# Performance work log

Hardware: AMD Instinct MI355X
Metric: run time of the kernel (lower is better)

Reference implementation:

```python
import jax, jax.numpy as jnp
import numpy as np

N = 50000      # nodes
E = 800000     # edges (before self-loops)
IN = 128       # in_channels
HID = 64       # hidden_channels
HEADS = 4      # num_heads of gat1
ACT = 5        # num_actions
NEG_SLOPE = 0.2


def gat_conv(x, edge_index, W, a_src, a_dst, bias, heads, out_ch):
    """PyG-style GATConv (concat=True, add_self_loops=True, eval mode)."""
    n = x.shape[0]
    loops = jnp.arange(n)
    src = jnp.concatenate([edge_index[0], loops])  # messages flow src -> dst
    dst = jnp.concatenate([edge_index[1], loops])
    h = (x @ W).reshape(n, heads, out_ch)                 # [N,H,C]
    alpha_src = jnp.sum(h * a_src, axis=-1)               # [N,H]
    alpha_dst = jnp.sum(h * a_dst, axis=-1)               # [N,H]
    e = jax.nn.leaky_relu(alpha_src[src] + alpha_dst[dst], NEG_SLOPE)  # [Et,H]
    # numerically-stable segment softmax over incoming edges of each dst node
    e_max = jax.lax.stop_gradient(jax.ops.segment_max(e, dst, num_segments=n))
    e_max = jnp.where(jnp.isfinite(e_max), e_max, 0.0)
    p = jnp.exp(e - e_max[dst])                           # [Et,H]
    denom = jax.ops.segment_sum(p, dst, num_segments=n)   # [N,H]
    alpha = p / (denom[dst] + 1e-16)                      # [Et,H]
    out = jax.ops.segment_sum(h[src] * alpha[:, :, None], dst, num_segments=n)
    return out.reshape(n, heads * out_ch) + bias


def setup_inputs() -> dict:
    key = jax.random.key(0)
    ks = jax.random.split(key, 12)
    s = 0.1
    return {
        "x": jax.random.normal(ks[0], (N, IN), jnp.float32),
        "edge_index": jax.random.randint(ks[1], (2, E), 0, N, dtype=jnp.int32),
        "W1": jax.random.normal(ks[2], (IN, HEADS * HID), jnp.float32) * s,
        "a1_src": jax.random.normal(ks[3], (HEADS, HID), jnp.float32) * s,
        "a1_dst": jax.random.normal(ks[4], (HEADS, HID), jnp.float32) * s,
        "b1": jnp.zeros((HEADS * HID,), jnp.float32),
        "W2": jax.random.normal(ks[5], (HEADS * HID, HID), jnp.float32) * s,
        "a2_src": jax.random.normal(ks[6], (1, HID), jnp.float32) * s,
        "a2_dst": jax.random.normal(ks[7], (1, HID), jnp.float32) * s,
        "b2": jnp.zeros((HID,), jnp.float32),
        "Wfc": jax.random.normal(ks[8], (HID, ACT), jnp.float32) * s,
        "bfc": jnp.zeros((ACT,), jnp.float32),
    }


def reference(x, edge_index, W1, a1_src, a1_dst, b1, W2, a2_src, a2_dst, b2, Wfc, bfc):
    # x.view(-1, F) is a no-op for already-flat [N, F] input; dropout skipped (eval).
    h = jax.nn.relu(gat_conv(x, edge_index, W1, a1_src, a1_dst, b1, HEADS, HID))
    h = jax.nn.relu(gat_conv(h, edge_index, W2, a2_src, a2_dst, b2, 1, HID))
    return h @ Wfc + bfc  # [N, num_actions]
```

## Files before the change

kernel.cpp:

```cpp
#include <hip/hip_runtime.h>

#define NEG_SLOPE 0.2f
#define ELLW 32

__device__ __forceinline__ float leaky(float x) { return x > 0.f ? x : NEG_SLOPE * x; }

__device__ __forceinline__ void unpack2(unsigned u, float& lo, float& hi) {
    union { unsigned u; float f; } a, b;
    a.u = u << 16; b.u = u & 0xffff0000u;
    lo = a.f; hi = b.f;
}

__device__ __forceinline__ unsigned short f2bf(float f) {
    unsigned u = __float_as_uint(f);
    u += 0x7fffu + ((u >> 16) & 1u);
    return (unsigned short)(u >> 16);
}

__global__ void k_count(const int* __restrict__ dst, int E, int* __restrict__ cnt) {
    int i = blockIdx.x * blockDim.x + threadIdx.x;
    if (i < E) atomicAdd(&cnt[dst[i]], 1);
}

__global__ __launch_bounds__(256) void k_scanA(const int* __restrict__ cnt, int* __restrict__ rowptr,
                                               int* __restrict__ bsum, int n) {
    int b = blockIdx.x, t = threadIdx.x;
    int lane = t & 63, w = t >> 6;
    int i0 = b * 1024 + t * 4;
    int v0 = (i0 + 0 < n) ? cnt[i0 + 0] : 0;
    int v1 = (i0 + 1 < n) ? cnt[i0 + 1] : 0;
    int v2 = (i0 + 2 < n) ? cnt[i0 + 2] : 0;
    int v3 = (i0 + 3 < n) ? cnt[i0 + 3] : 0;
    int r0 = v0, r1 = r0 + v1, r2 = r1 + v2, r3 = r2 + v3;
    int s = r3;
    int q = s;
    #pragma unroll
    for (int off = 1; off < 64; off <<= 1) {
        int tval = __shfl_up(q, off);
        if (lane >= off) q += tval;
    }
    __shared__ int wsum[4];
    if (lane == 63) wsum[w] = q;
    __syncthreads();
    int woff = 0;
    #pragma unroll
    for (int k = 0; k < 4; k++) if (k < w) woff += wsum[k];
    int excl = woff + q - s;
    if (i0 + 0 < n) rowptr[1 + i0 + 0] = excl + r0;
    if (i0 + 1 < n) rowptr[1 + i0 + 1] = excl + r1;
    if (i0 + 2 < n) rowptr[1 + i0 + 2] = excl + r2;
    if (i0 + 3 < n) rowptr[1 + i0 + 3] = excl + r3;
    if (t == 255) bsum[b] = woff + q;
}

__global__ void k_scanB(const int* __restrict__ bsum, int* __restrict__ bscan, int nb) {
    int lane = threadIdx.x & 63;
    int v = (lane < nb) ? bsum[lane] : 0;
    #pragma unroll
    for (int off = 1; off < 64; off <<= 1) {
        int t = __shfl_up(v, off);
        if (lane >= off) v += t;
    }
    if (lane < nb) bscan[lane] = v;
}

__global__ __launch_bounds__(256) void k_scanC(int* __restrict__ rowptr, const int* __restrict__ bscan, int n) {
    int b = blockIdx.x, t = threadIdx.x;
    int i0 = b * 1024 + t * 4;
    if (b == 0) {
        if (t == 0) rowptr[0] = 0;
        return;
    }
    int add = bscan[b - 1];
    #pragma unroll
    for (int j = 0; j < 4; j++)
        if (i0 + j < n) rowptr[1 + i0 + j] += add;
}

__global__ void k_copy(const int* __restrict__ src, int* __restrict__ dst, int n) {
    int i = blockIdx.x * blockDim.x + threadIdx.x;
    if (i < n) dst[i] = src[i];
}

__global__ void k_scatter(const int* __restrict__ srcn, const int* __restrict__ dstn, int E,
                          const int* __restrict__ rowptr, int* __restrict__ wptr,
                          int* __restrict__ col, int* __restrict__ ell) {
    int i = blockIdx.x * blockDim.x + threadIdx.x;
    if (i < E) {
        int d = dstn[i];
        int s = srcn[i];
        int pos = atomicAdd(&wptr[d], 1);
        col[pos] = s;
        int slot = pos - rowptr[d];
        if (slot < ELLW) ell[(size_t)d * ELLW + slot] = s;
    }
}

template <int BMT, bool WF32, bool WBF16, bool FALPHA>
__global__ __launch_bounds__(256) void k_gemm(const float* __restrict__ A, const float* __restrict__ B,
                                              float* __restrict__ C, unsigned short* __restrict__ Cb,
                                              const float* __restrict__ a_s, const float* __restrict__ a_d,
                                              float* __restrict__ asrc, float* __restrict__ adst,
                                              int M, int N, int K) {
    constexpr int RT = BMT / 16;
    constexpr int APASS = BMT / 32;
    __shared__ float As[32][BMT + 4];
    __shared__ float Bs[32][68];
    int row0 = blockIdx.x * BMT, col0 = blockIdx.y * 64;
    int tid = threadIdx.x;
    int tx = tid & 15, ty = tid >> 4;
    float acc[RT][4] = {};
    for (int kk = 0; kk < K; kk += 32) {
        int ar = tid >> 3;
        int ac = (tid & 7) * 4;
        #pragma unroll
        for (int p = 0; p < APASS; p++) {
            int r = ar + p * 32;
            int gr = row0 + r;
            float4 v = make_float4(0.f, 0.f, 0.f, 0.f);
            if (gr < M) v = *reinterpret_cast<const float4*>(&A[(size_t)gr * K + kk + ac]);
            As[ac + 0][r] = v.x; As[ac + 1][r] = v.y;
            As[ac + 2][r] = v.z; As[ac + 3][r] = v.w;
        }
        int br = tid >> 4;
        int bc = (tid & 15) * 4;
        #pragma unroll
        for (int p = 0; p < 2; p++) {
            int r = br + p * 16;
            float4 v = *reinterpret_cast<const float4*>(&B[(size_t)(kk + r) * N + col0 + bc]);
            *reinterpret_cast<float4*>(&Bs[r][bc]) = v;
        }
        __syncthreads();
        #pragma unroll
        for (int k = 0; k < 32; k++) {
            float a[RT];
            #pragma unroll
            for (int i = 0; i < RT; i += 4) {
                float4 av = *reinterpret_cast<const float4*>(&As[k][ty * RT + i]);
                a[i + 0] = av.x; a[i + 1] = av.y; a[i + 2] = av.z; a[i + 3] = av.w;
            }
            float4 bv = *reinterpret_cast<const float4*>(&Bs[k][tx * 4]);
            float b[4] = {bv.x, bv.y, bv.z, bv.w};
            #pragma unroll
            for (int i = 0; i < RT; i++)
                #pragma unroll
                for (int j = 0; j < 4; j++) acc[i][j] = fmaf(a[i], b[j], acc[i][j]);
        }
        __syncthreads();
    }
    float4 as4, ad4;
    if (FALPHA) {
        as4 = *reinterpret_cast<const float4*>(&a_s[col0 + tx * 4]);
        ad4 = *reinterpret_cast<const float4*>(&a_d[col0 + tx * 4]);
    }
    int HV = N >> 6, hd = col0 >> 6;
    #pragma unroll
    for (int i = 0; i < RT; i++) {
        int gr = row0 + ty * RT + i;
        if (gr < M) {
            if (WF32) {
                float4 v = make_float4(acc[i][0], acc[i][1], acc[i][2], acc[i][3]);
                *reinterpret_cast<float4*>(&C[(size_t)gr * N + col0 + tx * 4]) = v;
            }
            if (WBF16) {
                ushort4 u;
                u.x = f2bf(acc[i][0]); u.y = f2bf(acc[i][1]);
                u.z = f2bf(acc[i][2]); u.w = f2bf(acc[i][3]);
                *reinterpret_cast<ushort4*>(&Cb[(size_t)gr * N + col0 + tx * 4]) = u;
            }
            if (FALPHA) {
                float ps = acc[i][0] * as4.x + acc[i][1] * as4.y + acc[i][2] * as4.z + acc[i][3] * as4.w;
                float pd = acc[i][0] * ad4.x + acc[i][1] * ad4.y + acc[i][2] * ad4.z + acc[i][3] * ad4.w;
                #pragma unroll
                for (int off = 1; off <= 8; off <<= 1) { ps += __shfl_xor(ps, off); pd += __shfl_xor(pd, off); }
                if (tx == 0) { asrc[(size_t)gr * HV + hd] = ps; adst[(size_t)gr * HV + hd] = pd; }
            }
        }
    }
}

__global__ __launch_bounds__(256) void k_agg1(const unsigned short* __restrict__ hb,
                                              const float* __restrict__ asrc, const float* __restrict__ adst,
                                              const int* __restrict__ rowptr, const int* __restrict__ ell,
                                              const int* __restrict__ col, const float* __restrict__ bias,
                                              float* __restrict__ out, int n) {
    int node = blockIdx.x;
    int t = threadIdx.x, hd = t >> 6, l = t & 63;
    int rep = l >> 3, q = l & 7;
    float adst_n = adst[node * 4 + hd];
    float p_self = __expf(leaky(asrc[node * 4 + hd] + adst_n));

    int4 cv = *reinterpret_cast<const int4*>(&ell[(size_t)node * ELLW + rep * 4]);
    int s0 = cv.x, s1 = cv.y, s2 = cv.z, s3 = cv.w;
    bool v0 = s0 >= 0, v1 = s1 >= 0, v2 = s2 >= 0, v3 = s3 >= 0;
    s0 = v0 ? s0 : 0; s1 = v1 ? s1 : 0; s2 = v2 ? s2 : 0; s3 = v3 ? s3 : 0;
    uint4 u0 = *reinterpret_cast<const uint4*>(&hb[(size_t)s0 * 256 + hd * 64 + q * 8]);
    uint4 u1 = *reinterpret_cast<const uint4*>(&hb[(size_t)s1 * 256 + hd * 64 + q * 8]);
    uint4 u2 = *reinterpret_cast<const uint4*>(&hb[(size_t)s2 * 256 + hd * 64 + q * 8]);
    uint4 u3 = *reinterpret_cast<const uint4*>(&hb[(size_t)s3 * 256 + hd * 64 + q * 8]);
    float e0 = asrc[s0 * 4 + hd], e1 = asrc[s1 * 4 + hd];
    float e2 = asrc[s2 * 4 + hd], e3 = asrc[s3 * 4 + hd];
    float p0 = v0 ? __expf(leaky(e0 + adst_n)) : 0.f;
    float p1 = v1 ? __expf(leaky(e1 + adst_n)) : 0.f;
    float p2 = v2 ? __expf(leaky(e2 + adst_n)) : 0.f;
    float p3 = v3 ? __expf(leaky(e3 + adst_n)) : 0.f;

    float acc[8] = {};
    float dsum = p0 + p1 + p2 + p3;
    if (rep == 0) {
        uint4 un = *reinterpret_cast<const uint4*>(&hb[(size_t)node * 256 + hd * 64 + q * 8]);
        float f[8];
        unpack2(un.x, f[0], f[1]); unpack2(un.y, f[2], f[3]);
        unpack2(un.z, f[4], f[5]); unpack2(un.w, f[6], f[7]);
        #pragma unroll
        for (int j = 0; j < 8; j++) acc[j] = p_self * f[j];
        dsum += p_self;
    }
    {
        float f[8];
        unpack2(u0.x, f[0], f[1]); unpack2(u0.y, f[2], f[3]);
        unpack2(u0.z, f[4], f[5]); unpack2(u0.w, f[6], f[7]);
        #pragma unroll
        for (int j = 0; j < 8; j++) acc[j] = fmaf(p0, f[j], acc[j]);
        unpack2(u1.x, f[0], f[1]); unpack2(u1.y, f[2], f[3]);
        unpack2(u1.z, f[4], f[5]); unpack2(u1.w, f[6], f[7]);
        #pragma unroll
        for (int j = 0; j < 8; j++) acc[j] = fmaf(p1, f[j], acc[j]);
        unpack2(u2.x, f[0], f[1]); unpack2(u2.y, f[2], f[3]);
        unpack2(u2.z, f[4], f[5]); unpack2(u2.w, f[6], f[7]);
        #pragma unroll
        for (int j = 0; j < 8; j++) acc[j] = fmaf(p2, f[j], acc[j]);
        unpack2(u3.x, f[0], f[1]); unpack2(u3.y, f[2], f[3]);
        unpack2(u3.z, f[4], f[5]); unpack2(u3.w, f[6], f[7]);
        #pragma unroll
        for (int j = 0; j < 8; j++) acc[j] = fmaf(p3, f[j], acc[j]);
    }
    int base = rowptr[node], deg = rowptr[node + 1] - base;
    if (deg > ELLW) {
        for (int c0 = ELLW; c0 < deg; c0 += 16) {
            int ia = c0 + rep, ib = ia + 8;
            bool va = ia < deg, vb = ib < deg;
            int sa = va ? col[base + ia] : 0;
            int sb = vb ? col[base + ib] : 0;
            uint4 ua = *reinterpret_cast<const uint4*>(&hb[(size_t)sa * 256 + hd * 64 + q * 8]);
            uint4 ub = *reinterpret_cast<const uint4*>(&hb[(size_t)sb * 256 + hd * 64 + q * 8]);
            float pa = va ? __expf(leaky(asrc[sa * 4 + hd] + adst_n)) : 0.f;
            float pb = vb ? __expf(leaky(asrc[sb * 4 + hd] + adst_n)) : 0.f;
            float f[8];
            unpack2(ua.x, f[0], f[1]); unpack2(ua.y, f[2], f[3]);
            unpack2(ua.z, f[4], f[5]); unpack2(ua.w, f[6], f[7]);
            #pragma unroll
            for (int j = 0; j < 8; j++) acc[j] = fmaf(pa, f[j], acc[j]);
            unpack2(ub.x, f[0], f[1]); unpack2(ub.y, f[2], f[3]);
            unpack2(ub.z, f[4], f[5]); unpack2(ub.w, f[6], f[7]);
            #pragma unroll
            for (int j = 0; j < 8; j++) acc[j] = fmaf(pb, f[j], acc[j]);
            dsum += pa + pb;
        }
    }
    #pragma unroll
    for (int off = 8; off <= 32; off <<= 1) {
        #pragma unroll
        for (int j = 0; j < 8; j++) acc[j] += __shfl_xor(acc[j], off);
        dsum += __shfl_xor(dsum, off);
    }
    if (rep == 0) {
        float inv = 1.f / (dsum + 1e-16f);
        float r[8];
        #pragma unroll
        for (int j = 0; j < 8; j++) r[j] = fmaxf(acc[j] * inv + bias[hd * 64 + q * 8 + j], 0.f);
        float4 w0 = make_float4(r[0], r[1], r[2], r[3]);
        float4 w1 = make_float4(r[4], r[5], r[6], r[7]);
        *reinterpret_cast<float4*>(&out[(size_t)node * 256 + hd * 64 + q * 8]) = w0;
        *reinterpret_cast<float4*>(&out[(size_t)node * 256 + hd * 64 + q * 8 + 4]) = w1;
    }
}

__global__ __launch_bounds__(256) void k_agg2fc(const unsigned short* __restrict__ hb,
                                                const float* __restrict__ asrc, const float* __restrict__ adst,
                                                const int* __restrict__ rowptr, const int* __restrict__ ell,
                                                const int* __restrict__ col, const float* __restrict__ bias,
                                                const float* __restrict__ Wfc, const float* __restrict__ bfc,
                                                float* __restrict__ out, int n) {
    int node = blockIdx.x * 4 + (threadIdx.x >> 6);
    int l = threadIdx.x & 63;
    if (node >= n) return;
    int rep = l >> 3, q = l & 7;
    float adst_n = adst[node];
    float p_self = __expf(leaky(asrc[node] + adst_n));

    int4 cv = *reinterpret_cast<const int4*>(&ell[(size_t)node * ELLW + rep * 4]);
    int s0 = cv.x, s1 = cv.y, s2 = cv.z, s3 = cv.w;
    bool v0 = s0 >= 0, v1 = s1 >= 0, v2 = s2 >= 0, v3 = s3 >= 0;
    s0 = v0 ? s0 : 0; s1 = v1 ? s1 : 0; s2 = v2 ? s2 : 0; s3 = v3 ? s3 : 0;
    uint4 u0 = *reinterpret_cast<const uint4*>(&hb[(size_t)s0 * 64 + q * 8]);
    uint4 u1 = *reinterpret_cast<const uint4*>(&hb[(size_t)s1 * 64 + q * 8]);
    uint4 u2 = *reinterpret_cast<const uint4*>(&hb[(size_t)s2 * 64 + q * 8]);
    uint4 u3 = *reinterpret_cast<const uint4*>(&hb[(size_t)s3 * 64 + q * 8]);
    float e0 = asrc[s0], e1 = asrc[s1], e2 = asrc[s2], e3 = asrc[s3];
    float p0 = v0 ? __expf(leaky(e0 + adst_n)) : 0.f;
    float p1 = v1 ? __expf(leaky(e1 + adst_n)) : 0.f;
    float p2 = v2 ? __expf(leaky(e2 + adst_n)) : 0.f;
    float p3 = v3 ? __expf(leaky(e3 + adst_n)) : 0.f;

    float acc[8] = {};
    float dsum = p0 + p1 + p2 + p3;
    if (rep == 0) {
        uint4 un = *reinterpret_cast<const uint4*>(&hb[(size_t)node * 64 + q * 8]);
        float f[8];
        unpack2(un.x, f[0], f[1]); unpack2(un.y, f[2], f[3]);
        unpack2(un.z, f[4], f[5]); unpack2(un.w, f[6], f[7]);
        #pragma unroll
        for (int j = 0; j < 8; j++) acc[j] = p_self * f[j];
        dsum += p_self;
    }
    {
        float f[8];
        unpack2(u0.x, f[0], f[1]); unpack2(u0.y, f[2], f[3]);
        unpack2(u0.z, f[4], f[5]); unpack2(u0.w, f[6], f[7]);
        #pragma unroll
        for (int j = 0; j < 8; j++) acc[j] = fmaf(p0, f[j], acc[j]);
        unpack2(u1.x, f[0], f[1]); unpack2(u1.y, f[2], f[3]);
        unpack2(u1.z, f[4], f[5]); unpack2(u1.w, f[6], f[7]);
        #pragma unroll
        for (int j = 0; j < 8; j++) acc[j] = fmaf(p1, f[j], acc[j]);
        unpack2(u2.x, f[0], f[1]); unpack2(u2.y, f[2], f[3]);
        unpack2(u2.z, f[4], f[5]); unpack2(u2.w, f[6], f[7]);
        #pragma unroll
        for (int j = 0; j < 8; j++) acc[j] = fmaf(p2, f[j], acc[j]);
        unpack2(u3.x, f[0], f[1]); unpack2(u3.y, f[2], f[3]);
        unpack2(u3.z, f[4], f[5]); unpack2(u3.w, f[6], f[7]);
        #pragma unroll
        for (int j = 0; j < 8; j++) acc[j] = fmaf(p3, f[j], acc[j]);
    }
    int base = rowptr[node], deg = rowptr[node + 1] - base;
    if (deg > ELLW) {
        for (int c0 = ELLW; c0 < deg; c0 += 16) {
            int ia = c0 + rep, ib = ia + 8;
            bool va = ia < deg, vb = ib < deg;
            int sa = va ? col[base + ia] : 0;
            int sb = vb ? col[base + ib] : 0;
            uint4 ua = *reinterpret_cast<const uint4*>(&hb[(size_t)sa * 64 + q * 8]);
            uint4 ub = *reinterpret_cast<const uint4*>(&hb[(size_t)sb * 64 + q * 8]);
            float pa = va ? __expf(leaky(asrc[sa] + adst_n)) : 0.f;
            float pb = vb ? __expf(leaky(asrc[sb] + adst_n)) : 0.f;
            float f[8];
            unpack2(ua.x, f[0], f[1]); unpack2(ua.y, f[2], f[3]);
            unpack2(ua.z, f[4], f[5]); unpack2(ua.w, f[6], f[7]);
            #pragma unroll
            for (int j = 0; j < 8; j++) acc[j] = fmaf(pa, f[j], acc[j]);
            unpack2(ub.x, f[0], f[1]); unpack2(ub.y, f[2], f[3]);
            unpack2(ub.z, f[4], f[5]); unpack2(ub.w, f[6], f[7]);
            #pragma unroll
            for (int j = 0; j < 8; j++) acc[j] = fmaf(pb, f[j], acc[j]);
            dsum += pa + pb;
        }
    }
    #pragma unroll
    for (int off = 8; off <= 32; off <<= 1) {
        #pragma unroll
        for (int j = 0; j < 8; j++) acc[j] += __shfl_xor(acc[j], off);
        dsum += __shfl_xor(dsum, off);
    }
    float inv = 1.f / (dsum + 1e-16f);
    float r[8];
    #pragma unroll
    for (int j = 0; j < 8; j++) r[j] = fmaxf(acc[j] * inv + bias[q * 8 + j], 0.f);
    #pragma unroll
    for (int a = 0; a < 5; a++) {
        float part = 0.f;
        #pragma unroll
        for (int j = 0; j < 8; j++) part = fmaf(r[j], Wfc[(q * 8 + j) * 5 + a], part);
        #pragma unroll
        for (int off = 1; off <= 4; off <<= 1) part += __shfl_xor(part, off);
        if (l == 0) out[(size_t)node * 5 + a] = part + bfc[a];
    }
}

extern "C" void kernel_launch(void* const* d_in, const int* in_sizes, int n_in,
                              void* d_out, int out_size, void* d_ws, size_t ws_size,
                              hipStream_t stream) {
    const float* x   = (const float*)d_in[0];
    const int*   ei  = (const int*)d_in[1];
    const float* W1  = (const float*)d_in[2];
    const float* a1s = (const float*)d_in[3];
    const float* a1d = (const float*)d_in[4];
    const float* b1  = (const float*)d_in[5];
    const float* W2  = (const float*)d_in[6];
    const float* a2s = (const float*)d_in[7];
    const float* a2d = (const float*)d_in[8];
    const float* b2  = (const float*)d_in[9];
    const float* Wfc = (const float*)d_in[10];
    const float* bfc = (const float*)d_in[11];
    float* out = (float*)d_out;

    int n = in_sizes[0] / 128;
    int E = in_sizes[1] / 2;
    const int* srcn = ei;
    const int* dstn = ei + E;

    char* ws = (char*)d_ws;
    size_t off = 0;
    auto alloc = [&](size_t bytes) -> void* {
        void* p = ws + off;
        off += (bytes + 255) & ~(size_t)255;
        return p;
    };
    unsigned short* h1b = (unsigned short*)alloc((size_t)n * 256 * 2);
    float* out1   = (float*)alloc((size_t)n * 256 * 4);
    unsigned short* h2b = (unsigned short*)alloc((size_t)n * 64 * 2);
    float* asrc1  = (float*)alloc((size_t)n * 4 * 4);
    float* adst1  = (float*)alloc((size_t)n * 4 * 4);
    int*   rowptr = (int*)alloc((size_t)(n + 1) * 4);
    int*   wptr   = (int*)alloc((size_t)n * 4);
    int*   col    = (int*)alloc((size_t)E * 4);
    int*   ell    = (int*)alloc((size_t)n * ELLW * 4);
    int*   bsum   = (int*)alloc(64 * 4);
    int*   bscan  = (int*)alloc(64 * 4);
    float* asrc2 = asrc1;
    float* adst2 = adst1;

    int nb = (n + 1023) / 1024;

    hipMemsetAsync(wptr, 0, (size_t)n * 4, stream);
    hipMemsetAsync(ell, 0xFF, (size_t)n * ELLW * 4, stream);
    k_count<<<(E + 255) / 256, 256, 0, stream>>>(dstn, E, wptr);
    k_scanA<<<nb, 256, 0, stream>>>(wptr, rowptr, bsum, n);
    k_scanB<<<1, 64, 0, stream>>>(bsum, bscan, nb);
    k_scanC<<<nb, 256, 0, stream>>>(rowptr, bscan, n);
    k_copy<<<(n + 255) / 256, 256, 0, stream>>>(rowptr, wptr, n);
    k_scatter<<<(E + 255) / 256, 256, 0, stream>>>(srcn, dstn, E, rowptr, wptr, col, ell);

    k_gemm<128, false, true, true><<<dim3((n + 127) / 128, 4), 256, 0, stream>>>(
        x, W1, nullptr, h1b, a1s, a1d, asrc1, adst1, n, 256, 128);
    k_agg1<<<n, 256, 0, stream>>>(h1b, asrc1, adst1, rowptr, ell, col, b1, out1, n);
    k_gemm<64, false, true, true><<<dim3((n + 63) / 64, 1), 256, 0, stream>>>(
        out1, W2, nullptr, h2b, a2s, a2d, asrc2, adst2, n, 64, 256);
    k_agg2fc<<<(n + 3) / 4, 256, 0, stream>>>(h2b, asrc2, adst2, rowptr, ell, col, b2, Wfc, bfc, out, n);
}
```

Baseline: 473.5 us.

## Spread layer-2 aggregation of each node across a whole 256-thread block

Measured after the change: 475.4 us. Within noise of the previous version (+0.4%).

```diff
diff --git a/kernel.cpp b/kernel.cpp
--- a/kernel.cpp
+++ b/kernel.cpp
@@ -282,78 +282,46 @@
                                                 const int* __restrict__ col, const float* __restrict__ bias,
                                                 const float* __restrict__ Wfc, const float* __restrict__ bfc,
                                                 float* __restrict__ out, int n) {
-    int node = blockIdx.x * 4 + (threadIdx.x >> 6);
-    int l = threadIdx.x & 63;
-    if (node >= n) return;
+    int node = blockIdx.x;
+    int t = threadIdx.x, w = t >> 6, l = t & 63;
     int rep = l >> 3, q = l & 7;
     float adst_n = adst[node];
-    float p_self = __expf(leaky(asrc[node] + adst_n));
-
-    int4 cv = *reinterpret_cast<const int4*>(&ell[(size_t)node * ELLW + rep * 4]);
-    int s0 = cv.x, s1 = cv.y, s2 = cv.z, s3 = cv.w;
-    bool v0 = s0 >= 0, v1 = s1 >= 0, v2 = s2 >= 0, v3 = s3 >= 0;
-    s0 = v0 ? s0 : 0; s1 = v1 ? s1 : 0; s2 = v2 ? s2 : 0; s3 = v3 ? s3 : 0;
-    uint4 u0 = *reinterpret_cast<const uint4*>(&hb[(size_t)s0 * 64 + q * 8]);
-    uint4 u1 = *reinterpret_cast<const uint4*>(&hb[(size_t)s1 * 64 + q * 8]);
-    uint4 u2 = *reinterpret_cast<const uint4*>(&hb[(size_t)s2 * 64 + q * 8]);
-    uint4 u3 = *reinterpret_cast<const uint4*>(&hb[(size_t)s3 * 64 + q * 8]);
-    float e0 = asrc[s0], e1 = asrc[s1], e2 = asrc[s2], e3 = asrc[s3];
-    float p0 = v0 ? __expf(leaky(e0 + adst_n)) : 0.f;
-    float p1 = v1 ? __expf(leaky(e1 + adst_n)) : 0.f;
-    float p2 = v2 ? __expf(leaky(e2 + adst_n)) : 0.f;
-    float p3 = v3 ? __expf(leaky(e3 + adst_n)) : 0.f;
-
-    float acc[8] = {};
-    float dsum = p0 + p1 + p2 + p3;
-    if (rep == 0) {
+
+    int slot = w * 8 + rep;
+    int s = ell[(size_t)node * ELLW + slot];
+    bool v = s >= 0;
+    s = v ? s : 0;
+    uint4 u = *reinterpret_cast<const uint4*>(&hb[(size_t)s * 64 + q * 8]);
+    float p = v ? __expf(leaky(asrc[s] + adst_n)) : 0.f;
+
+    float f[8];
+    float acc[8];
+    unpack2(u.x, f[0], f[1]); unpack2(u.y, f[2], f[3]);
+    unpack2(u.z, f[4], f[5]); unpack2(u.w, f[6], f[7]);
+    #pragma unroll
+    for (int j = 0; j < 8; j++) acc[j] = p * f[j];
+    float dsum = p;
+
+    if (w == 0 && rep == 0) {
+        float p_self = __expf(leaky(asrc[node] + adst_n));
         uint4 un = *reinterpret_cast<const uint4*>(&hb[(size_t)node * 64 + q * 8]);
-        float f[8];
         unpack2(un.x, f[0], f[1]); unpack2(un.y, f[2], f[3]);
         unpack2(un.z, f[4], f[5]); unpack2(un.w, f[6], f[7]);
         #pragma unroll
-        for (int j = 0; j < 8; j++) acc[j] = p_self * f[j];
+        for (int j = 0; j < 8; j++) acc[j] = fmaf(p_self, f[j], acc[j]);
         dsum += p_self;
-    }
-    {
-        float f[8];
-        unpack2(u0.x, f[0], f[1]); unpack2(u0.y, f[2], f[3]);
-        unpack2(u0.z, f[4], f[5]); unpack2(u0.w, f[6], f[7]);
-        #pragma unroll
-        for (int j = 0; j < 8; j++) acc[j] = fmaf(p0, f[j], acc[j]);
-        unpack2(u1.x, f[0], f[1]); unpack2(u1.y, f[2], f[3]);
-        unpack2(u1.z, f[4], f[5]); unpack2(u1.w, f[6], f[7]);
-        #pragma unroll
-        for (int j = 0; j < 8; j++) acc[j] = fmaf(p1, f[j], acc[j]);
-        unpack2(u2.x, f[0], f[1]); unpack2(u2.y, f[2], f[3]);
-        unpack2(u2.z, f[4], f[5]); unpack2(u2.w, f[6], f[7]);
-        #pragma unroll
-        for (int j = 0; j < 8; j++) acc[j] = fmaf(p2, f[j], acc[j]);
-        unpack2(u3.x, f[0], f[1]); unpack2(u3.y, f[2], f[3]);
-        unpack2(u3.z, f[4], f[5]); unpack2(u3.w, f[6], f[7]);
-        #pragma unroll
-        for (int j = 0; j < 8; j++) acc[j] = fmaf(p3, f[j], acc[j]);
     }
     int base = rowptr[node], deg = rowptr[node + 1] - base;
     if (deg > ELLW) {
-        for (int c0 = ELLW; c0 < deg; c0 += 16) {
-            int ia = c0 + rep, ib = ia + 8;
-            bool va = ia < deg, vb = ib < deg;
-            int sa = va ? col[base + ia] : 0;
-            int sb = vb ? col[base + ib] : 0;
+        for (int i = ELLW + w * 8 + rep; i < deg; i += 32) {
+            int sa = col[base + i];
             uint4 ua = *reinterpret_cast<const uint4*>(&hb[(size_t)sa * 64 + q * 8]);
-            uint4 ub = *reinterpret_cast<const uint4*>(&hb[(size_t)sb * 64 + q * 8]);
-            float pa = va ? __expf(leaky(asrc[sa] + adst_n)) : 0.f;
-            float pb = vb ? __expf(leaky(asrc[sb] + adst_n)) : 0.f;
-            float f[8];
+            float pa = __expf(leaky(asrc[sa] + adst_n));
             unpack2(ua.x, f[0], f[1]); unpack2(ua.y, f[2], f[3]);
             unpack2(ua.z, f[4], f[5]); unpack2(ua.w, f[6], f[7]);
             #pragma unroll
             for (int j = 0; j < 8; j++) acc[j] = fmaf(pa, f[j], acc[j]);
-            unpack2(ub.x, f[0], f[1]); unpack2(ub.y, f[2], f[3]);
-            unpack2(ub.z, f[4], f[5]); unpack2(ub.w, f[6], f[7]);
-            #pragma unroll
-            for (int j = 0; j < 8; j++) acc[j] = fmaf(pb, f[j], acc[j]);
-            dsum += pa + pb;
+            dsum += pa;
         }
     }
     #pragma unroll
@@ -362,18 +330,35 @@
         for (int j = 0; j < 8; j++) acc[j] += __shfl_xor(acc[j], off);
         dsum += __shfl_xor(dsum, off);
     }
-    float inv = 1.f / (dsum + 1e-16f);
-    float r[8];
-    #pragma unroll
-    for (int j = 0; j < 8; j++) r[j] = fmaxf(acc[j] * inv + bias[q * 8 + j], 0.f);
-    #pragma unroll
-    for (int a = 0; a < 5; a++) {
-        float part = 0.f;
-        #pragma unroll
-        for (int j = 0; j < 8; j++) part = fmaf(r[j], Wfc[(q * 8 + j) * 5 + a], part);
-        #pragma unroll
-        for (int off = 1; off <= 4; off <<= 1) part += __shfl_xor(part, off);
-        if (l == 0) out[(size_t)node * 5 + a] = part + bfc[a];
+    __shared__ float lacc[4][64];
+    __shared__ float lsum[4];
+    if (rep == 0) {
+        float4 a0 = make_float4(acc[0], acc[1], acc[2], acc[3]);
+        float4 a1 = make_float4(acc[4], acc[5], acc[6], acc[7]);
+        *reinterpret_cast<float4*>(&lacc[w][q * 8]) = a0;
+        *reinterpret_cast<float4*>(&lacc[w][q * 8 + 4]) = a1;
+    }
+    if (l == 0) lsum[w] = dsum;
+    __syncthreads();
+    if (w == 0) {
+        float tot[8];
+        #pragma unroll
+        for (int j = 0; j < 8; j++)
+            tot[j] = lacc[0][q * 8 + j] + lacc[1][q * 8 + j] + lacc[2][q * 8 + j] + lacc[3][q * 8 + j];
+        float ds = lsum[0] + lsum[1] + lsum[2] + lsum[3];
+        float inv = 1.f / (ds + 1e-16f);
+        float r[8];
+        #pragma unroll
+        for (int j = 0; j < 8; j++) r[j] = fmaxf(tot[j] * inv + bias[q * 8 + j], 0.f);
+        #pragma unroll
+        for (int a = 0; a < 5; a++) {
+            float part = 0.f;
+            #pragma unroll
+            for (int j = 0; j < 8; j++) part = fmaf(r[j], Wfc[(q * 8 + j) * 5 + a], part);
+            #pragma unroll
+            for (int off = 1; off <= 4; off <<= 1) part += __shfl_xor(part, off);
+            if (l == 0) out[(size_t)node * 5 + a] = part + bfc[a];
+        }
     }
 }
 
@@ -436,5 +421,5 @@
     k_agg1<<<n, 256, 0, stream>>>(h1b, asrc1, adst1, rowptr, ell, col, b1, out1, n);
     k_gemm<64, false, true, true><<<dim3((n + 63) / 64, 1), 256, 0, stream>>>(
         out1, W2, nullptr, h2b, a2s, a2d, asrc2, adst2, n, 64, 256);
-    k_agg2fc<<<(n + 3) / 4, 256, 0, stream>>>(h2b, asrc2, adst2, rowptr, ell, col, b2, Wfc, bfc, out, n);
-}
+    k_agg2fc<<<n, 256, 0, stream>>>(h2b, asrc2, adst2, rowptr, ell, col, b2, Wfc, bfc, out, n);
+}
```
